# Kernel optimization log

Hardware: AMD Instinct MI355X
Metric: run time of the kernel (lower is better)

## Reference

```python
import math
import jax, jax.numpy as jnp
import numpy as np

D_MODEL = 1024
NUM_HEADS = 16
HEAD_DIM = D_MODEL // NUM_HEADS
B, T = 4, 2048


def _get_slopes(n_heads: int) -> np.ndarray:
    def pow2_slopes(n):
        start = 2 ** (-(2 ** (-(math.log2(n) - 3))))
        return [start * start ** i for i in range(n)]
    if math.log2(n_heads).is_integer():
        return np.array(pow2_slopes(n_heads), dtype=np.float32)
    closest = 2 ** math.floor(math.log2(n_heads))
    slopes = pow2_slopes(closest)
    slopes += pow2_slopes(2 * closest)[0::2][: n_heads - closest]
    return np.array(slopes[:n_heads], dtype=np.float32)


def setup_inputs() -> dict:
    key = jax.random.key(0)
    ks = jax.random.split(key, 6)
    init = 0.02
    return {
        "x": jax.random.normal(ks[0], (B, T, D_MODEL), dtype=jnp.float32),
        "wq": jax.random.normal(ks[1], (D_MODEL, D_MODEL), dtype=jnp.float32) * init,
        "wk": jax.random.normal(ks[2], (D_MODEL, D_MODEL), dtype=jnp.float32) * init,
        "wv": jax.random.normal(ks[3], (D_MODEL, D_MODEL), dtype=jnp.float32) * init,
        "wo": jax.random.normal(ks[4], (D_MODEL, D_MODEL), dtype=jnp.float32) * init,
        "bo": jnp.zeros((D_MODEL,), dtype=jnp.float32),
    }


def reference(x, wq, wk, wv, wo, bo):
    Bx, Tx, _ = x.shape
    H, Dh = NUM_HEADS, HEAD_DIM
    scale = math.sqrt(Dh)
    # nn.Linear: y = x @ W^T
    q = (x @ wq.T).reshape(Bx, Tx, H, Dh).transpose(0, 2, 1, 3)  # (B,H,T,D)
    k = (x @ wk.T).reshape(Bx, Tx, H, Dh).transpose(0, 2, 1, 3)
    v = (x @ wv.T).reshape(Bx, Tx, H, Dh).transpose(0, 2, 1, 3)
    attn = jnp.einsum("bhqd,bhkd->bhqk", q, k) / scale
    # ALiBi bias: -slope * |i - j|, symmetric distance as in the source
    pos = jnp.arange(Tx)
    dist = -jnp.abs(pos[None, :] - pos[:, None]).astype(jnp.float32)  # (T,T)
    slopes = jnp.asarray(_get_slopes(H))  # (H,)
    attn = attn + slopes[None, :, None, None] * dist[None, None, :, :]
    attn = jax.nn.softmax(attn, axis=-1)
    out = jnp.einsum("bhqk,bhkd->bhqd", attn, v)
    out = out.transpose(0, 2, 1, 3).reshape(Bx, Tx, H * Dh)
    return out @ wo.T + bo
```

## Files before the change

### kernel.cpp

```cpp
#include <hip/hip_runtime.h>

#define DMODEL 1024
#define NHEADS 16
#define HDIM   64
#define BB     4
#define TT     2048

typedef __attribute__((ext_vector_type(8))) short bf16x8;
typedef __attribute__((ext_vector_type(4))) short bf16x4;
typedef __attribute__((ext_vector_type(4))) float f32x4;

#if __has_builtin(__builtin_amdgcn_exp2f)
#define EXP2(x) __builtin_amdgcn_exp2f(x)
#else
#define EXP2(x) __expf(0.69314718f * (x))
#endif

#define C1SCALE 0.18033688f

__device__ inline void async16(const void* g, void* l) {
  __builtin_amdgcn_global_load_lds(
      (const __attribute__((address_space(1))) unsigned int*)g,
      (__attribute__((address_space(3))) unsigned int*)l,
      16, 0, 0);
}

__device__ inline unsigned short f2bf(float x) {
  union { float f; unsigned int u; } c; c.f = x;
  unsigned int r = (c.u + 0x7FFFu + ((c.u >> 16) & 1u)) >> 16;
  return (unsigned short)r;
}

__device__ inline unsigned int pkbf(float x, float y) {
  union { float f; unsigned int u; } a, b; a.f = x; b.f = y;
  return __builtin_amdgcn_perm(b.u, a.u, 0x07060302u);
}

__global__ __launch_bounds__(256) void cvt_all(
    const float* __restrict__ x,  const float* __restrict__ wq,
    const float* __restrict__ wk, const float* __restrict__ wv,
    const float* __restrict__ wo,
    unsigned short* __restrict__ xb, unsigned short* __restrict__ wqkvb,
    unsigned short* __restrict__ wob)
{
  int bid = blockIdx.x;
  const float* src; unsigned short* dst; size_t off;
  if (bid < 8192) { src = x; dst = xb; off = (size_t)bid * 1024; }
  else {
    int w = (bid - 8192) >> 10, r = (bid - 8192) & 1023;
    off = (size_t)r * 1024;
    if (w == 0)      { src = wq; dst = wqkvb; }
    else if (w == 1) { src = wk; dst = wqkvb + 1048576; }
    else if (w == 2) { src = wv; dst = wqkvb + 2097152; }
    else             { src = wo; dst = wob; }
  }
  size_t i = off + threadIdx.x * 4;
  float4 v = *(const float4*)(src + i);
  ushort4 o;
  o.x = f2bf(v.x); o.y = f2bf(v.y); o.z = f2bf(v.z); o.w = f2bf(v.w);
  *(ushort4*)(dst + i) = o;
}

__global__ __launch_bounds__(512, 4) void gemm_qkv(
    const unsigned short* __restrict__ A, const unsigned short* __restrict__ W,
    unsigned short* __restrict__ qw, unsigned short* __restrict__ kw,
    unsigned short* __restrict__ vtw)
{
  __shared__ unsigned short As[2][128 * 64];
  __shared__ unsigned short Bs[2][128 * 64];
  const int tid  = threadIdx.x;
  const int lane = tid & 63;
  const int wave = tid >> 6;
  const int lo   = lane & 15, q4 = lane >> 4;
  const int lo7  = lane & 7;
  const int wm   = wave & 3, wn = wave >> 2;
  const int m0 = blockIdx.x * 128;
  const int nb = blockIdx.y;
  const int n0 = nb * 128;
  const int mid = nb >> 3;

  f32x4 acc[2][4] = {};

  auto stage = [&](int k0, int buf) {
#pragma unroll
    for (int i = 0; i < 2; ++i) {
      int ci = i * 512 + tid;
      int row = ci >> 3;
      int c = (ci & 7) ^ (row & 7);
      async16(A + (size_t)(m0 + row) * DMODEL + k0 + c * 8, (char*)As[buf] + ci * 16);
      async16(W + (size_t)(n0 + row) * DMODEL + k0 + c * 8, (char*)Bs[buf] + ci * 16);
    }
  };

  stage(0, 0);
  for (int it = 0; it < DMODEL / 64; ++it) {
    const int buf = it & 1;
    __syncthreads();
    if (it + 1 < DMODEL / 64) stage((it + 1) * 64, buf ^ 1);
#pragma unroll
    for (int hh = 0; hh < 2; ++hh) {
      bf16x8 af[2], bf[4];
#pragma unroll
      for (int mi = 0; mi < 2; ++mi)
        af[mi] = *(const bf16x8*)&As[buf][(wm * 32 + mi * 16 + lo) * 64 + ((hh * 4 + q4) ^ lo7) * 8];
#pragma unroll
      for (int ni = 0; ni < 4; ++ni)
        bf[ni] = *(const bf16x8*)&Bs[buf][(wn * 64 + ni * 16 + lo) * 64 + ((hh * 4 + q4) ^ lo7) * 8];
#pragma unroll
      for (int mi = 0; mi < 2; ++mi)
#pragma unroll
        for (int ni = 0; ni < 4; ++ni)
          acc[mi][ni] = __builtin_amdgcn_mfma_f32_16x16x32_bf16(af[mi], bf[ni], acc[mi][ni], 0, 0, 0);
    }
  }

  unsigned short* dst = (mid == 0) ? qw : (mid == 1) ? kw : vtw;
  const float sc = (mid == 0) ? C1SCALE : 1.0f;
#pragma unroll
  for (int mi = 0; mi < 2; ++mi) {
#pragma unroll
    for (int ni = 0; ni < 4; ++ni) {
#pragma unroll
      for (int r = 0; r < 4; ++r) {
        int m = m0 + wm * 32 + mi * 16 + q4 * 4 + r;
        int nl = ((nb & 7) * 128) + wn * 64 + ni * 16 + lo;
        float v = acc[mi][ni][r] * sc;
        int b = m >> 11, t = m & (TT - 1);
        int h = nl >> 6, d = nl & 63;
        if (mid == 2)
          dst[(((size_t)(b * NHEADS + h)) * HDIM + d) * TT + t] = f2bf(v);
        else
          dst[(((size_t)(b * NHEADS + h)) * TT + t) * HDIM + d] = f2bf(v);
      }
    }
  }
}

__global__ __launch_bounds__(512, 4) void gemm_out(
    const unsigned short* __restrict__ A, const unsigned short* __restrict__ W,
    const float* __restrict__ bias, float* __restrict__ C)
{
  __shared__ unsigned short As[2][128 * 64];
  __shared__ unsigned short Bs[2][128 * 64];
  const int tid  = threadIdx.x;
  const int lane = tid & 63;
  const int wave = tid >> 6;
  const int lo   = lane & 15, q4 = lane >> 4;
  const int lo7  = lane & 7;
  const int wm   = wave & 3, wn = wave >> 2;
  const int m0 = blockIdx.x * 128, n0 = blockIdx.y * 128;

  f32x4 acc[2][4] = {};

  auto stage = [&](int k0, int buf) {
#pragma unroll
    for (int i = 0; i < 2; ++i) {
      int ci = i * 512 + tid;
      int row = ci >> 3;
      int c = (ci & 7) ^ (row & 7);
      async16(A + (size_t)(m0 + row) * DMODEL + k0 + c * 8, (char*)As[buf] + ci * 16);
      async16(W + (size_t)(n0 + row) * DMODEL + k0 + c * 8, (char*)Bs[buf] + ci * 16);
    }
  };

  stage(0, 0);
  for (int it = 0; it < DMODEL / 64; ++it) {
    const int buf = it & 1;
    __syncthreads();
    if (it + 1 < DMODEL / 64) stage((it + 1) * 64, buf ^ 1);
#pragma unroll
    for (int hh = 0; hh < 2; ++hh) {
      bf16x8 af[2], bf[4];
#pragma unroll
      for (int mi = 0; mi < 2; ++mi)
        af[mi] = *(const bf16x8*)&As[buf][(wm * 32 + mi * 16 + lo) * 64 + ((hh * 4 + q4) ^ lo7) * 8];
#pragma unroll
      for (int ni = 0; ni < 4; ++ni)
        bf[ni] = *(const bf16x8*)&Bs[buf][(wn * 64 + ni * 16 + lo) * 64 + ((hh * 4 + q4) ^ lo7) * 8];
#pragma unroll
      for (int mi = 0; mi < 2; ++mi)
#pragma unroll
        for (int ni = 0; ni < 4; ++ni)
          acc[mi][ni] = __builtin_amdgcn_mfma_f32_16x16x32_bf16(af[mi], bf[ni], acc[mi][ni], 0, 0, 0);
    }
  }

#pragma unroll
  for (int mi = 0; mi < 2; ++mi)
#pragma unroll
    for (int ni = 0; ni < 4; ++ni)
#pragma unroll
      for (int r = 0; r < 4; ++r) {
        int m = m0 + wm * 32 + mi * 16 + q4 * 4 + r;
        int n = n0 + wn * 64 + ni * 16 + lo;
        C[(size_t)m * DMODEL + n] = acc[mi][ni][r] + bias[n];
      }
}

__global__ __launch_bounds__(256, 4) void attn_kernel(
    const unsigned short* __restrict__ Q, const unsigned short* __restrict__ K,
    const unsigned short* __restrict__ Vt, unsigned short* __restrict__ O)
{
  __shared__ unsigned short Ks[2][64 * 64];
  __shared__ unsigned short Vs[2][64 * 64];

  const int tid = threadIdx.x, lane = tid & 63, wave = tid >> 6;
  const int lo = lane & 15, q4 = lane >> 4;
  const int lo7 = lane & 7;
  const int bid = blockIdx.x;
  const int h  = (int)((0x3201765489ABFEDCull >> ((bid >> 6) * 4)) & 15);
  const int qb = bid & 15;
  const int b  = (bid >> 4) & 3;
  const int bh = b * NHEADS + h;
  const float slopeL = exp2f(-0.5f * (float)(h + 1)) * 1.44269504f;
  const int q0 = qb * 128;
  const int wq0 = q0 + wave * 32;

  const int D = (int)(19.407f * exp2f(0.5f * (float)(h + 1)));
  int tlo = q0 - D;
  const int ktlo = (tlo <= 0) ? 0 : (tlo >> 6);
  int thi = (q0 + 127 + D) >> 6;
  const int kthi = (thi > TT / 64 - 1) ? TT / 64 - 1 : thi;

  bf16x8 qf[2][2];
#pragma unroll
  for (int m = 0; m < 2; ++m)
#pragma unroll
    for (int hh = 0; hh < 2; ++hh)
      qf[m][hh] = *(const bf16x8*)(Q + ((size_t)bh * TT + wq0 + m * 16 + lo) * HDIM + hh * 32 + q4 * 8);

  bf16x8 ones8;
  {
    short o = (lo == 0) ? (short)0x3F80 : (short)0;
    ones8 = bf16x8{o, o, o, o, o, o, o, o};
  }

  f32x4 Oacc[2][4];
  f32x4 lacc[2];
#pragma unroll
  for (int m = 0; m < 2; ++m) {
    lacc[m] = f32x4{0.f, 0.f, 0.f, 0.f};
#pragma unroll
    for (int nd = 0; nd < 4; ++nd) Oacc[m][nd] = f32x4{0.f, 0.f, 0.f, 0.f};
  }

  float eb[2][4];
#pragma unroll
  for (int m = 0; m < 2; ++m)
#pragma unroll
    for (int r = 0; r < 4; ++r)
      eb[m][r] = (float)(wq0 + m * 16 + lo - q4 * 4 - r);

  const unsigned short* kbh = K + (size_t)bh * TT * HDIM;
  const unsigned short* vbh = Vt + (size_t)bh * HDIM * TT;

  auto stage = [&](int kt, int buf) {
#pragma unroll
    for (int i = 0; i < 2; ++i) {
      int ci = i * 256 + tid;
      int row = ci >> 3;
      int c = (ci & 7) ^ (row & 7);
      async16(kbh + (size_t)(kt * 64 + row) * HDIM + c * 8, (char*)Ks[buf] + ci * 16);
      async16(vbh + (size_t)row * TT + kt * 64 + c * 8,     (char*)Vs[buf] + ci * 16);
    }
  };

  stage(ktlo, 0);

  for (int kt = ktlo; kt <= kthi; ++kt) {
    const int buf = (kt - ktlo) & 1;
    __syncthreads();
    if (kt < kthi) stage(kt + 1, buf ^ 1);

#pragma unroll
    for (int pp = 0; pp < 2; ++pp) {
      unsigned int ua[2][2], ub[2][2];
#pragma unroll
      for (int hns = 0; hns < 2; ++hns) {
        const int ns = pp * 2 + hns;
        const int krow = (ns * 16 + lo) * 64;
        bf16x8 kf0 = *(const bf16x8*)&Ks[buf][krow + ((q4) ^ lo7) * 8];
        bf16x8 kf1 = *(const bf16x8*)&Ks[buf][krow + ((4 + q4) ^ lo7) * 8];
        const float kb = (float)(kt * 64 + ns * 16);
#pragma unroll
        for (int m = 0; m < 2; ++m) {
          f32x4 a = {0.f, 0.f, 0.f, 0.f};
          __builtin_amdgcn_s_setprio(1);
          a = __builtin_amdgcn_mfma_f32_16x16x32_bf16(kf0, qf[m][0], a, 0, 0, 0);
          a = __builtin_amdgcn_mfma_f32_16x16x32_bf16(kf1, qf[m][1], a, 0, 0, 0);
          __builtin_amdgcn_s_setprio(0);
          float pv[4];
#pragma unroll
          for (int r = 0; r < 4; ++r) {
            float w = eb[m][r] - kb;
            pv[r] = EXP2(fmaf(-slopeL, fabsf(w), a[r]));
          }
          ua[hns][m] = pkbf(pv[0], pv[1]);
          ub[hns][m] = pkbf(pv[2], pv[3]);
        }
      }

      bf16x8 paf[2];
#pragma unroll
      for (int m = 0; m < 2; ++m) {
        unsigned int w0 = ua[0][m], w2 = ua[1][m];
        unsigned int w1 = ub[0][m], w3 = ub[1][m];
        asm("v_permlane32_swap_b32 %0, %1" : "+v"(w0), "+v"(w2));
        asm("v_permlane16_swap_b32 %0, %1" : "+v"(w0), "+v"(w2));
        asm("v_permlane32_swap_b32 %0, %1" : "+v"(w1), "+v"(w3));
        asm("v_permlane16_swap_b32 %0, %1" : "+v"(w1), "+v"(w3));
        union { bf16x8 v; unsigned int u[4]; } U;
        U.u[0] = w0; U.u[1] = w1; U.u[2] = w2; U.u[3] = w3;
        paf[m] = U.v;
      }

#pragma unroll
      for (int nd = 0; nd < 4; ++nd) {
        const int row = nd * 16 + lo;
        bf16x8 vb = *(const bf16x8*)&Vs[buf][row * 64 + ((pp * 4 + q4) ^ lo7) * 8];
        __builtin_amdgcn_s_setprio(1);
#pragma unroll
        for (int m = 0; m < 2; ++m)
          Oacc[m][nd] = __builtin_amdgcn_mfma_f32_16x16x32_bf16(paf[m], vb, Oacc[m][nd], 0, 0, 0);
        __builtin_amdgcn_s_setprio(0);
      }
#pragma unroll
      for (int m = 0; m < 2; ++m)
        lacc[m] = __builtin_amdgcn_mfma_f32_16x16x32_bf16(paf[m], ones8, lacc[m], 0, 0, 0);
    }
  }

#pragma unroll
  for (int m = 0; m < 2; ++m)
#pragma unroll
    for (int r = 0; r < 4; ++r) {
      float l = __shfl(lacc[m][r], lane & 48);
      float inv = 1.f / l;
      int t = wq0 + m * 16 + q4 * 4 + r;
#pragma unroll
      for (int nd = 0; nd < 4; ++nd) {
        int d = nd * 16 + lo;
        O[((size_t)(b * TT + t)) * DMODEL + h * HDIM + d] = f2bf(Oacc[m][nd][r] * inv);
      }
    }
}

extern "C" void kernel_launch(void* const* d_in, const int* in_sizes, int n_in,
                              void* d_out, int out_size, void* d_ws, size_t ws_size,
                              hipStream_t stream) {
  const float* x  = (const float*)d_in[0];
  const float* wq = (const float*)d_in[1];
  const float* wk = (const float*)d_in[2];
  const float* wv = (const float*)d_in[3];
  const float* wo = (const float*)d_in[4];
  const float* bo = (const float*)d_in[5];
  float* out = (float*)d_out;

  char* ws = (char*)d_ws;
  const size_t seg  = (size_t)BB * TT * DMODEL * sizeof(unsigned short);
  const size_t wseg = (size_t)DMODEL * DMODEL * sizeof(unsigned short);
  unsigned short* qw    = (unsigned short*)(ws);
  unsigned short* kw    = (unsigned short*)(ws + seg);
  unsigned short* vtw   = (unsigned short*)(ws + 2 * seg);
  unsigned short* ow    = (unsigned short*)(ws + 3 * seg);
  unsigned short* xb    = (unsigned short*)(ws + 4 * seg);
  unsigned short* wqkvb = (unsigned short*)(ws + 5 * seg);
  unsigned short* wob   = (unsigned short*)(ws + 5 * seg + 3 * wseg);

  cvt_all<<<dim3(8192 + 4096), dim3(256), 0, stream>>>(x, wq, wk, wv, wo, xb, wqkvb, wob);

  gemm_qkv<<<dim3(64, 24), dim3(512), 0, stream>>>(xb, wqkvb, qw, kw, vtw);

  attn_kernel<<<dim3(BB * NHEADS * (TT / 128)), dim3(256), 0, stream>>>(qw, kw, vtw, ow);

  gemm_out<<<dim3(64, 8), dim3(512), 0, stream>>>(ow, wob, bo, out);
}
```

Before: 244.1 us.

## Restructure projection GEMMs to 256x128 tiles with triple-buffered async pipeline

Measured after the change: 268.3 us. 9.9% more time.

```diff
diff --git a/kernel.cpp b/kernel.cpp
--- a/kernel.cpp
+++ b/kernel.cpp
@@ -61,70 +61,109 @@
   *(ushort4*)(dst + i) = o;
 }
 
-__global__ __launch_bounds__(512, 4) void gemm_qkv(
+__global__ __launch_bounds__(512, 2) void gemm_qkv(
     const unsigned short* __restrict__ A, const unsigned short* __restrict__ W,
     unsigned short* __restrict__ qw, unsigned short* __restrict__ kw,
     unsigned short* __restrict__ vtw)
 {
-  __shared__ unsigned short As[2][128 * 64];
-  __shared__ unsigned short Bs[2][128 * 64];
+  __shared__ unsigned short As[3][256 * 64];
+  __shared__ unsigned short Bs[3][128 * 64];
   const int tid  = threadIdx.x;
   const int lane = tid & 63;
   const int wave = tid >> 6;
   const int lo   = lane & 15, q4 = lane >> 4;
   const int lo7  = lane & 7;
-  const int wm   = wave & 3, wn = wave >> 2;
-  const int m0 = blockIdx.x * 128;
+  const int wm   = wave >> 2;
+  const int wn   = wave & 3;
+  const int m0 = blockIdx.x * 256;
   const int nb = blockIdx.y;
   const int n0 = nb * 128;
   const int mid = nb >> 3;
 
-  f32x4 acc[2][4] = {};
-
-  auto stage = [&](int k0, int buf) {
-#pragma unroll
-    for (int i = 0; i < 2; ++i) {
-      int ci = i * 512 + tid;
-      int row = ci >> 3;
-      int c = (ci & 7) ^ (row & 7);
-      async16(A + (size_t)(m0 + row) * DMODEL + k0 + c * 8, (char*)As[buf] + ci * 16);
-      async16(W + (size_t)(n0 + row) * DMODEL + k0 + c * 8, (char*)Bs[buf] + ci * 16);
-    }
-  };
-
-  stage(0, 0);
-  for (int it = 0; it < DMODEL / 64; ++it) {
-    const int buf = it & 1;
-    __syncthreads();
-    if (it + 1 < DMODEL / 64) stage((it + 1) * 64, buf ^ 1);
-#pragma unroll
-    for (int hh = 0; hh < 2; ++hh) {
-      bf16x8 af[2], bf[4];
-#pragma unroll
-      for (int mi = 0; mi < 2; ++mi)
-        af[mi] = *(const bf16x8*)&As[buf][(wm * 32 + mi * 16 + lo) * 64 + ((hh * 4 + q4) ^ lo7) * 8];
-#pragma unroll
-      for (int ni = 0; ni < 4; ++ni)
-        bf[ni] = *(const bf16x8*)&Bs[buf][(wn * 64 + ni * 16 + lo) * 64 + ((hh * 4 + q4) ^ lo7) * 8];
-#pragma unroll
-      for (int mi = 0; mi < 2; ++mi)
-#pragma unroll
-        for (int ni = 0; ni < 4; ++ni)
-          acc[mi][ni] = __builtin_amdgcn_mfma_f32_16x16x32_bf16(af[mi], bf[ni], acc[mi][ni], 0, 0, 0);
-    }
+  f32x4 acc[8][2] = {};
+
+  auto stageA = [&](int k0, int buf, int i) {
+    int ci = i * 512 + tid;
+    int row = ci >> 3;
+    int c = (ci & 7) ^ (row & 7);
+    async16(A + (size_t)(m0 + row) * DMODEL + k0 + c * 8, (char*)As[buf] + ci * 16);
+  };
+  auto stageB = [&](int k0, int buf, int i) {
+    int ci = i * 512 + tid;
+    int row = ci >> 3;
+    int c = (ci & 7) ^ (row & 7);
+    async16(W + (size_t)(n0 + row) * DMODEL + k0 + c * 8, (char*)Bs[buf] + ci * 16);
+  };
+  auto stage_all = [&](int k0, int buf) {
+    stageA(k0, buf, 0); stageA(k0, buf, 1); stageA(k0, buf, 2); stageA(k0, buf, 3);
+    stageB(k0, buf, 0); stageB(k0, buf, 1);
+  };
+
+  stage_all(0, 0);
+  stage_all(64, 1);
+
+  const int NT = DMODEL / 64;
+  int cur = 0;
+  for (int t = 0; t < NT; ++t) {
+    if (t + 1 < NT) asm volatile("s_waitcnt vmcnt(6)" ::: "memory");
+    else            asm volatile("s_waitcnt vmcnt(0)" ::: "memory");
+    __builtin_amdgcn_s_barrier();
+
+    const unsigned short* Ab = As[cur];
+    const unsigned short* Bb = Bs[cur];
+    const int nxt = (cur + 2 >= 3) ? cur - 1 : cur + 2;
+    const int k2 = (t + 2) * 64;
+    const bool pre = (t + 2 < NT);
+
+    bf16x8 bfr[2][2];
+#pragma unroll
+    for (int p = 0; p < 4; ++p) {
+      bf16x8 af[2][2];
+#pragma unroll
+      for (int j = 0; j < 2; ++j)
+#pragma unroll
+        for (int kk = 0; kk < 2; ++kk)
+          af[j][kk] = *(const bf16x8*)&Ab[(wm * 128 + (p * 2 + j) * 16 + lo) * 64 + ((kk * 4 + q4) ^ lo7) * 8];
+      if (p == 0) {
+#pragma unroll
+        for (int nf = 0; nf < 2; ++nf)
+#pragma unroll
+          for (int kk = 0; kk < 2; ++kk)
+            bfr[nf][kk] = *(const bf16x8*)&Bb[(wn * 32 + nf * 16 + lo) * 64 + ((kk * 4 + q4) ^ lo7) * 8];
+      }
+      if (pre) {
+        if      (p == 0) { stageA(k2, nxt, 0); stageA(k2, nxt, 1); }
+        else if (p == 1) { stageA(k2, nxt, 2); stageA(k2, nxt, 3); }
+        else if (p == 2) { stageB(k2, nxt, 0); stageB(k2, nxt, 1); }
+      }
+      __builtin_amdgcn_s_barrier();
+      asm volatile("s_waitcnt lgkmcnt(0)" ::: "memory");
+      __builtin_amdgcn_sched_barrier(0);
+      __builtin_amdgcn_s_setprio(1);
+#pragma unroll
+      for (int j = 0; j < 2; ++j)
+#pragma unroll
+        for (int nf = 0; nf < 2; ++nf)
+#pragma unroll
+          for (int kk = 0; kk < 2; ++kk)
+            acc[p * 2 + j][nf] = __builtin_amdgcn_mfma_f32_16x16x32_bf16(af[j][kk], bfr[nf][kk], acc[p * 2 + j][nf], 0, 0, 0);
+      __builtin_amdgcn_s_setprio(0);
+      __builtin_amdgcn_s_barrier();
+    }
+    cur = (cur + 1 == 3) ? 0 : cur + 1;
   }
 
   unsigned short* dst = (mid == 0) ? qw : (mid == 1) ? kw : vtw;
   const float sc = (mid == 0) ? C1SCALE : 1.0f;
 #pragma unroll
-  for (int mi = 0; mi < 2; ++mi) {
-#pragma unroll
-    for (int ni = 0; ni < 4; ++ni) {
+  for (int mf = 0; mf < 8; ++mf) {
+#pragma unroll
+    for (int nf = 0; nf < 2; ++nf) {
 #pragma unroll
       for (int r = 0; r < 4; ++r) {
-        int m = m0 + wm * 32 + mi * 16 + q4 * 4 + r;
-        int nl = ((nb & 7) * 128) + wn * 64 + ni * 16 + lo;
-        float v = acc[mi][ni][r] * sc;
+        int m = m0 + wm * 128 + mf * 16 + q4 * 4 + r;
+        int nl = ((nb & 7) * 128) + wn * 32 + nf * 16 + lo;
+        float v = acc[mf][nf][r] * sc;
         int b = m >> 11, t = m & (TT - 1);
         int h = nl >> 6, d = nl & 63;
         if (mid == 2)
@@ -136,64 +175,103 @@
   }
 }
 
-__global__ __launch_bounds__(512, 4) void gemm_out(
+__global__ __launch_bounds__(512, 2) void gemm_out(
     const unsigned short* __restrict__ A, const unsigned short* __restrict__ W,
     const float* __restrict__ bias, float* __restrict__ C)
 {
-  __shared__ unsigned short As[2][128 * 64];
-  __shared__ unsigned short Bs[2][128 * 64];
+  __shared__ unsigned short As[3][256 * 64];
+  __shared__ unsigned short Bs[3][128 * 64];
   const int tid  = threadIdx.x;
   const int lane = tid & 63;
   const int wave = tid >> 6;
   const int lo   = lane & 15, q4 = lane >> 4;
   const int lo7  = lane & 7;
-  const int wm   = wave & 3, wn = wave >> 2;
-  const int m0 = blockIdx.x * 128, n0 = blockIdx.y * 128;
-
-  f32x4 acc[2][4] = {};
-
-  auto stage = [&](int k0, int buf) {
-#pragma unroll
-    for (int i = 0; i < 2; ++i) {
-      int ci = i * 512 + tid;
-      int row = ci >> 3;
-      int c = (ci & 7) ^ (row & 7);
-      async16(A + (size_t)(m0 + row) * DMODEL + k0 + c * 8, (char*)As[buf] + ci * 16);
-      async16(W + (size_t)(n0 + row) * DMODEL + k0 + c * 8, (char*)Bs[buf] + ci * 16);
-    }
-  };
-
-  stage(0, 0);
-  for (int it = 0; it < DMODEL / 64; ++it) {
-    const int buf = it & 1;
-    __syncthreads();
-    if (it + 1 < DMODEL / 64) stage((it + 1) * 64, buf ^ 1);
-#pragma unroll
-    for (int hh = 0; hh < 2; ++hh) {
-      bf16x8 af[2], bf[4];
-#pragma unroll
-      for (int mi = 0; mi < 2; ++mi)
-        af[mi] = *(const bf16x8*)&As[buf][(wm * 32 + mi * 16 + lo) * 64 + ((hh * 4 + q4) ^ lo7) * 8];
-#pragma unroll
-      for (int ni = 0; ni < 4; ++ni)
-        bf[ni] = *(const bf16x8*)&Bs[buf][(wn * 64 + ni * 16 + lo) * 64 + ((hh * 4 + q4) ^ lo7) * 8];
-#pragma unroll
-      for (int mi = 0; mi < 2; ++mi)
-#pragma unroll
-        for (int ni = 0; ni < 4; ++ni)
-          acc[mi][ni] = __builtin_amdgcn_mfma_f32_16x16x32_bf16(af[mi], bf[ni], acc[mi][ni], 0, 0, 0);
-    }
-  }
-
-#pragma unroll
-  for (int mi = 0; mi < 2; ++mi)
-#pragma unroll
-    for (int ni = 0; ni < 4; ++ni)
+  const int wm   = wave >> 2;
+  const int wn   = wave & 3;
+  const int m0 = blockIdx.x * 256, n0 = blockIdx.y * 128;
+
+  f32x4 acc[8][2] = {};
+
+  auto stageA = [&](int k0, int buf, int i) {
+    int ci = i * 512 + tid;
+    int row = ci >> 3;
+    int c = (ci & 7) ^ (row & 7);
+    async16(A + (size_t)(m0 + row) * DMODEL + k0 + c * 8, (char*)As[buf] + ci * 16);
+  };
+  auto stageB = [&](int k0, int buf, int i) {
+    int ci = i * 512 + tid;
+    int row = ci >> 3;
+    int c = (ci & 7) ^ (row & 7);
+    async16(W + (size_t)(n0 + row) * DMODEL + k0 + c * 8, (char*)Bs[buf] + ci * 16);
+  };
+  auto stage_all = [&](int k0, int buf) {
+    stageA(k0, buf, 0); stageA(k0, buf, 1); stageA(k0, buf, 2); stageA(k0, buf, 3);
+    stageB(k0, buf, 0); stageB(k0, buf, 1);
+  };
+
+  stage_all(0, 0);
+  stage_all(64, 1);
+
+  const int NT = DMODEL / 64;
+  int cur = 0;
+  for (int t = 0; t < NT; ++t) {
+    if (t + 1 < NT) asm volatile("s_waitcnt vmcnt(6)" ::: "memory");
+    else            asm volatile("s_waitcnt vmcnt(0)" ::: "memory");
+    __builtin_amdgcn_s_barrier();
+
+    const unsigned short* Ab = As[cur];
+    const unsigned short* Bb = Bs[cur];
+    const int nxt = (cur + 2 >= 3) ? cur - 1 : cur + 2;
+    const int k2 = (t + 2) * 64;
+    const bool pre = (t + 2 < NT);
+
+    bf16x8 bfr[2][2];
+#pragma unroll
+    for (int p = 0; p < 4; ++p) {
+      bf16x8 af[2][2];
+#pragma unroll
+      for (int j = 0; j < 2; ++j)
+#pragma unroll
+        for (int kk = 0; kk < 2; ++kk)
+          af[j][kk] = *(const bf16x8*)&Ab[(wm * 128 + (p * 2 + j) * 16 + lo) * 64 + ((kk * 4 + q4) ^ lo7) * 8];
+      if (p == 0) {
+#pragma unroll
+        for (int nf = 0; nf < 2; ++nf)
+#pragma unroll
+          for (int kk = 0; kk < 2; ++kk)
+            bfr[nf][kk] = *(const bf16x8*)&Bb[(wn * 32 + nf * 16 + lo) * 64 + ((kk * 4 + q4) ^ lo7) * 8];
+      }
+      if (pre) {
+        if      (p == 0) { stageA(k2, nxt, 0); stageA(k2, nxt, 1); }
+        else if (p == 1) { stageA(k2, nxt, 2); stageA(k2, nxt, 3); }
+        else if (p == 2) { stageB(k2, nxt, 0); stageB(k2, nxt, 1); }
+      }
+      __builtin_amdgcn_s_barrier();
+      asm volatile("s_waitcnt lgkmcnt(0)" ::: "memory");
+      __builtin_amdgcn_sched_barrier(0);
+      __builtin_amdgcn_s_setprio(1);
+#pragma unroll
+      for (int j = 0; j < 2; ++j)
+#pragma unroll
+        for (int nf = 0; nf < 2; ++nf)
+#pragma unroll
+          for (int kk = 0; kk < 2; ++kk)
+            acc[p * 2 + j][nf] = __builtin_amdgcn_mfma_f32_16x16x32_bf16(af[j][kk], bfr[nf][kk], acc[p * 2 + j][nf], 0, 0, 0);
+      __builtin_amdgcn_s_setprio(0);
+      __builtin_amdgcn_s_barrier();
+    }
+    cur = (cur + 1 == 3) ? 0 : cur + 1;
+  }
+
+#pragma unroll
+  for (int mf = 0; mf < 8; ++mf)
+#pragma unroll
+    for (int nf = 0; nf < 2; ++nf)
 #pragma unroll
       for (int r = 0; r < 4; ++r) {
-        int m = m0 + wm * 32 + mi * 16 + q4 * 4 + r;
-        int n = n0 + wn * 64 + ni * 16 + lo;
-        C[(size_t)m * DMODEL + n] = acc[mi][ni][r] + bias[n];
+        int m = m0 + wm * 128 + mf * 16 + q4 * 4 + r;
+        int n = n0 + wn * 32 + nf * 16 + lo;
+        C[(size_t)m * DMODEL + n] = acc[mf][nf][r] + bias[n];
       }
 }
 
@@ -369,9 +447,9 @@
 
   cvt_all<<<dim3(8192 + 4096), dim3(256), 0, stream>>>(x, wq, wk, wv, wo, xb, wqkvb, wob);
 
-  gemm_qkv<<<dim3(64, 24), dim3(512), 0, stream>>>(xb, wqkvb, qw, kw, vtw);
+  gemm_qkv<<<dim3(32, 24), dim3(512), 0, stream>>>(xb, wqkvb, qw, kw, vtw);
 
   attn_kernel<<<dim3(BB * NHEADS * (TT / 128)), dim3(256), 0, stream>>>(qw, kw, vtw, ow);
 
-  gemm_out<<<dim3(64, 8), dim3(512), 0, stream>>>(ow, wob, bo, out);
-}
+  gemm_out<<<dim3(32, 8), dim3(512), 0, stream>>>(ow, wob, bo, out);
+}
```
